# Optimization experiments

Hardware: AMD Instinct MI355X
Metric: run time of the kernel (lower is better)

Reference implementation:

```python
import jax, jax.numpy as jnp
import numpy as np

HIDDEN = 768

def setup_inputs() -> dict:
    key = jax.random.key(0)
    ks = jax.random.split(key, 7)
    x = jax.random.normal(ks[0], (4, 4096, HIDDEN), dtype=jnp.float32)
    s = 1.0 / np.sqrt(HIDDEN)
    Wq = jax.random.uniform(ks[1], (HIDDEN, HIDDEN), minval=-s, maxval=s, dtype=jnp.float32)
    Wk = jax.random.uniform(ks[2], (HIDDEN, HIDDEN), minval=-s, maxval=s, dtype=jnp.float32)
    Wv = jax.random.uniform(ks[3], (HIDDEN, HIDDEN), minval=-s, maxval=s, dtype=jnp.float32)
    bq = jax.random.uniform(ks[4], (HIDDEN,), minval=-s, maxval=s, dtype=jnp.float32)
    bk = jax.random.uniform(ks[5], (HIDDEN,), minval=-s, maxval=s, dtype=jnp.float32)
    bv = jax.random.uniform(ks[6], (HIDDEN,), minval=-s, maxval=s, dtype=jnp.float32)
    return {"x": x, "Wq": Wq, "bq": bq, "Wk": Wk, "bk": bk, "Wv": Wv, "bv": bv}

def reference(x, Wq, bq, Wk, bk, Wv, bv):
    # q,k,v: [b, s, d]
    q = jnp.einsum('bsd,de->bse', x, Wq.T) + bq
    k = jnp.einsum('bsd,de->bse', x, Wk.T) + bk
    v = jnp.einsum('bsd,de->bse', x, Wv.T) + bv
    scale = 1.0 / jnp.sqrt(jnp.asarray(x.shape[-1], dtype=x.dtype))
    scores = jnp.einsum('bqd,bkd->bqk', q, k) * scale  # [b, s, s]
    attn = jax.nn.softmax(scores, axis=-1)
    return jnp.einsum('bqk,bkd->bqd', attn, v)
```

## Files before the change

kernel.cpp:

```cpp
#include <hip/hip_runtime.h>
#include <stdint.h>

typedef unsigned short u16;
typedef __attribute__((ext_vector_type(8))) short    bf16x8;
typedef __attribute__((ext_vector_type(4))) float    f32x4;

__device__ __forceinline__ u16 f2bf(float f) {
    unsigned u = __float_as_uint(f);
    u = (u + 0x7fffu + ((u >> 16) & 1u)) >> 16;
    return (u16)u;
}

__global__ __launch_bounds__(256) void cast_bf16_kernel(const float* __restrict__ in,
                                                        u16* __restrict__ out, int n4) {
    int i = blockIdx.x * 256 + threadIdx.x;
    if (i < n4) {
        float4 f = ((const float4*)in)[i];
        ushort4 o;
        o.x = f2bf(f.x); o.y = f2bf(f.y); o.z = f2bf(f.z); o.w = f2bf(f.w);
        ((ushort4*)out)[i] = o;
    }
}

__global__ __launch_bounds__(256) void cast3_bf16_kernel(const float* __restrict__ w0,
                                                         const float* __restrict__ w1,
                                                         const float* __restrict__ w2,
                                                         u16* __restrict__ out) {
    const float* src = (blockIdx.y == 0) ? w0 : (blockIdx.y == 1) ? w1 : w2;
    int i = blockIdx.x * 256 + threadIdx.x;
    float4 f = ((const float4*)src)[i];
    ushort4 o;
    o.x = f2bf(f.x); o.y = f2bf(f.y); o.z = f2bf(f.z); o.w = f2bf(f.w);
    ((ushort4*)out)[(size_t)blockIdx.y * 147456 + i] = o;
}

__global__ __launch_bounds__(256) void transpose_bf16_kernel(const u16* __restrict__ V,
                                                             u16* __restrict__ Vt,
                                                             float* __restrict__ rsum) {
    __shared__ u16 tile[32][33];
    const int t = threadIdx.x;
    if (blockIdx.x == 0 && blockIdx.z == 0) {
        int idx = blockIdx.y * 256 + t;
        if (idx < 16384) rsum[idx] = 0.f;
    }
    const size_t z = blockIdx.z;
    const u16* Vb  = V  + z * (size_t)4096 * 2304;
    u16*       Vtb = Vt + z * (size_t)768 * 4096;
    const int c0 = blockIdx.x * 32;
    const int r0 = blockIdx.y * 32;
    const int lr = t >> 3;
    const int lc = (t & 7) * 4;
    ushort4 in = *(const ushort4*)&Vb[(size_t)(r0 + lr) * 2304 + c0 + lc];
    tile[lr][lc + 0] = in.x; tile[lr][lc + 1] = in.y;
    tile[lr][lc + 2] = in.z; tile[lr][lc + 3] = in.w;
    __syncthreads();
    ushort4 o;
    o.x = tile[lc + 0][lr]; o.y = tile[lc + 1][lr];
    o.z = tile[lc + 2][lr]; o.w = tile[lc + 3][lr];
    *(ushort4*)&Vtb[(size_t)(c0 + lr) * 4096 + r0 + lc] = o;
}

template <int EPI, int WN, int NBX, int GRP, int NGRID, int NBY, int MINW>
__global__ __launch_bounds__(256, MINW) void gemm_bt_kernel(
        const u16* __restrict__ A, const u16* __restrict__ B, void* __restrict__ Cv,
        const float* __restrict__ b0, const float* __restrict__ b1, const float* __restrict__ b2,
        float* __restrict__ rs, float s2, int K,
        int lda, int ldb, int ldc, long batchA, long batchB, long batchC) {
    __shared__ __align__(16) u16 As[128 * 64];
    __shared__ __align__(16) u16 Bs[32 * WN * 64];

    constexpr int SPX = NGRID / (8 * NBX);
    const int lin = blockIdx.x;
    const int c = lin & 7, p = lin >> 3;
    const int bxi = p % GRP;
    const int rest = p / GRP;
    const int s = rest % SPX;
    const int g = rest / SPX;
    const int bx = g * GRP + bxi;
    const int strip = c * SPX + s;
    const int by = strip % NBY;
    const int bz = strip / NBY;

    const int t = threadIdx.x;
    const long z = bz;
    const u16* Ab = A + z * batchA + (long)by * 128 * lda;
    const u16* Bb = B + z * batchB + (long)bx * (32 * WN) * ldb;

    const int lane = t & 63;
    const int wave = t >> 6;
    const int wm = wave >> 1, wn = wave & 1;
    const int quad = lane >> 4;
    const int frow = lane & 15;
    const int cc0 = quad ^ (frow & 7);

    f32x4 acc[4][WN];
#pragma unroll
    for (int i = 0; i < 4; i++)
#pragma unroll
        for (int j = 0; j < WN; j++)
#pragma unroll
            for (int e = 0; e < 4; e++) acc[i][j][e] = 0.f;

    int srow[WN], scol[WN];
#pragma unroll
    for (int j = 0; j < WN; j++) {
        const int d = t + j * 256;
        srow[j] = d >> 3;
        scol[j] = ((d & 7) ^ (srow[j] & 7)) * 8;
    }

    bf16x8 ra[4], rb[WN];
#pragma unroll
    for (int j = 0; j < 4; j++)
        ra[j] = *(const bf16x8*)(Ab + (long)srow[j] * lda + scol[j]);
#pragma unroll
    for (int j = 0; j < WN; j++)
        rb[j] = *(const bf16x8*)(Bb + (long)srow[j] * ldb + scol[j]);

    for (int kt = 0; kt < K; kt += 64) {
#pragma unroll
        for (int j = 0; j < 4; j++)
            *(bf16x8*)&As[(t + j * 256) * 8] = ra[j];
#pragma unroll
        for (int j = 0; j < WN; j++)
            *(bf16x8*)&Bs[(t + j * 256) * 8] = rb[j];
        __syncthreads();

        if (kt + 64 < K) {
            const int kn = kt + 64;
#pragma unroll
            for (int j = 0; j < 4; j++)
                ra[j] = *(const bf16x8*)(Ab + (long)srow[j] * lda + kn + scol[j]);
#pragma unroll
            for (int j = 0; j < WN; j++)
                rb[j] = *(const bf16x8*)(Bb + (long)srow[j] * ldb + kn + scol[j]);
        }

#pragma unroll
        for (int kk = 0; kk < 2; kk++) {
            const int cc = (cc0 ^ (kk * 4)) * 8;
            bf16x8 bfr[WN];
#pragma unroll
            for (int j = 0; j < WN; j++)
                bfr[j] = *(const bf16x8*)&Bs[(wn * WN * 16 + j * 16 + frow) * 64 + cc];
#pragma unroll
            for (int i = 0; i < 4; i++) {
                bf16x8 af = *(const bf16x8*)&As[(wm * 64 + i * 16 + frow) * 64 + cc];
#pragma unroll
                for (int j = 0; j < WN; j++)
                    acc[i][j] = __builtin_amdgcn_mfma_f32_16x16x32_bf16(af, bfr[j], acc[i][j], 0, 0, 0);
            }
        }
        __syncthreads();
    }

    const int m_base = by * 128 + wm * 64;
    const int n_base = bx * (32 * WN) + wn * (16 * WN);

    if (EPI == 0) {
        const int seg = n_base / 768;
        const float* bp = (seg == 0) ? b0 : (seg == 1) ? b1 : b2;
        u16* C = (u16*)Cv + z * batchC;
#pragma unroll
        for (int j = 0; j < WN; j++) {
            const int col = n_base + j * 16 + frow;
            const float bb = bp[col - seg * 768];
#pragma unroll
            for (int i = 0; i < 4; i++) {
                const int row0 = m_base + i * 16 + quad * 4;
#pragma unroll
                for (int r = 0; r < 4; r++)
                    C[(long)(row0 + r) * ldc + col] = f2bf(acc[i][j][r] + bb);
            }
        }
    } else if (EPI == 1) {
        u16* C = (u16*)Cv + z * batchC;
        float rowpart[4][4];
#pragma unroll
        for (int i = 0; i < 4; i++)
#pragma unroll
            for (int r = 0; r < 4; r++) rowpart[i][r] = 0.f;
#pragma unroll
        for (int i = 0; i < 4; i++) {
            const int row0 = m_base + i * 16 + quad * 4;
#pragma unroll
            for (int j = 0; j < WN; j++) {
                const int col = n_base + j * 16 + frow;
#pragma unroll
                for (int r = 0; r < 4; r++) {
                    float e = exp2f(acc[i][j][r] * s2);
                    C[(long)(row0 + r) * ldc + col] = f2bf(e);
                    rowpart[i][r] += e;
                }
            }
        }
#pragma unroll
        for (int i = 0; i < 4; i++)
#pragma unroll
            for (int r = 0; r < 4; r++) {
                float v = rowpart[i][r];
                v += __shfl_xor(v, 1); v += __shfl_xor(v, 2);
                v += __shfl_xor(v, 4); v += __shfl_xor(v, 8);
                if (frow == 0)
                    atomicAdd(&rs[z * 4096 + m_base + i * 16 + quad * 4 + r], v);
            }
    } else {
        float* C = (float*)Cv + z * batchC;
#pragma unroll
        for (int i = 0; i < 4; i++) {
            const int row0 = m_base + i * 16 + quad * 4;
            float inv[4];
#pragma unroll
            for (int r = 0; r < 4; r++) inv[r] = 1.0f / rs[z * 4096 + row0 + r];
#pragma unroll
            for (int j = 0; j < WN; j++) {
                const int col = n_base + j * 16 + frow;
#pragma unroll
                for (int r = 0; r < 4; r++)
                    C[(long)(row0 + r) * ldc + col] = acc[i][j][r] * inv[r];
            }
        }
    }
}

__device__ __forceinline__ void gload16(const u16* src, u16* dst) {
    __builtin_amdgcn_global_load_lds((const __attribute__((address_space(1))) void*)src,
                                     (__attribute__((address_space(3))) void*)dst,
                                     16, 0, 0);
}

template <int EPI, int NBX, int NBY, int NT>
__global__ __launch_bounds__(512, 2) void gemm8_kernel(
        const u16* __restrict__ A, const u16* __restrict__ B, void* __restrict__ Cv,
        float* __restrict__ rs, float s2,
        int lda, int ldb, int ldc, long batchA, long batchB, long batchC) {
    static_assert(NT >= 3, "pipeline needs >=3 K-tiles");
    __shared__ __align__(16) u16 lds[2][4][8192];

    constexpr int NWG = NBX * NBY * 4;
    const int lin = blockIdx.x;
    const int swz = (lin & 7) * (NWG / 8) + (lin >> 3);
    const int bz  = swz / (NBX * NBY);
    const int rr_ = swz % (NBX * NBY);
    const int by  = rr_ / NBX, bx = rr_ % NBX;

    const int t_   = threadIdx.x;
    const int lane = t_ & 63;
    const int wave = t_ >> 6;
    const int wm = wave >> 2, wn = wave & 3;
    const int frow = lane & 15, quad = lane >> 4;

    const u16* Ab = A + (long)bz * batchA + (long)by * 256 * lda;
    const u16* Bb = B + (long)bz * batchB + (long)bx * 256 * ldb;

    const int srow = ((t_ >> 3) << 1) | ((t_ >> 2) & 1);
    const int scol = ((t_ & 3) ^ ((t_ >> 3) & 3)) * 8;
    const int dstu = wave * 512;

    const int rdoff = (frow >> 1) * 64
                    + ((frow & 1) * 4 + (quad ^ ((frow >> 1) & 3))) * 8;
    const int aoff = wm * 128 * 32 + rdoff;
    const int boff = wn * 64 * 32 + rdoff;

    f32x4 acc[8][4];
#pragma unroll
    for (int i = 0; i < 8; i++)
#pragma unroll
        for (int j = 0; j < 4; j++)
#pragma unroll
            for (int e = 0; e < 4; e++) acc[i][j][e] = 0.f;

    auto STAGE = [&](int buf, int reg, const u16* gb, int ld_, int kofs) {
#pragma unroll
        for (int j = 0; j < 2; ++j) {
            const u16* sp = gb + (long)(srow + j * 128) * ld_ + kofs + scol;
            gload16(sp, &lds[buf][reg][dstu + j * 4096]);
        }
    };

    STAGE(0, 2, Bb, ldb, 0);
    STAGE(0, 0, Ab, lda, 0);
    STAGE(0, 3, Bb, ldb, 32);
    STAGE(0, 1, Ab, lda, 32);
    STAGE(1, 2, Bb, ldb, 64);
    STAGE(1, 0, Ab, lda, 64);
    STAGE(1, 3, Bb, ldb, 96);
    asm volatile("s_waitcnt vmcnt(6)" ::: "memory");
    __builtin_amdgcn_s_barrier();

#define MFMA16(SUB)                                                              \
    __builtin_amdgcn_s_setprio(1);                                               \
    _Pragma("unroll")                                                            \
    for (int i = 0; i < 4; ++i)                                                  \
        _Pragma("unroll")                                                        \
        for (int j = 0; j < 4; ++j)                                              \
            acc[(SUB) * 4 + i][j] = __builtin_amdgcn_mfma_f32_16x16x32_bf16(     \
                a[i], b[j], acc[(SUB) * 4 + i][j], 0, 0, 0);                     \
    __builtin_amdgcn_s_setprio(0);

#pragma unroll 2
    for (int t = 0; t < NT; ++t) {
        const int cur = t & 1, nxt = cur ^ 1;
        const u16* A0 = (const u16*)lds[cur][0];
        const u16* A1 = (const u16*)lds[cur][1];
        const u16* B0 = (const u16*)lds[cur][2];
        const u16* B1 = (const u16*)lds[cur][3];
        bf16x8 a[4], b[4];

#pragma unroll
        for (int i = 0; i < 4; ++i) a[i] = *(const bf16x8*)&A0[aoff + i * 512];
#pragma unroll
        for (int j = 0; j < 4; ++j) b[j] = *(const bf16x8*)&B0[boff + j * 512];
        if (t + 1 < NT) STAGE(nxt, 1, Ab, lda, (t + 1) * 64 + 32);
        __builtin_amdgcn_s_barrier();
        asm volatile("s_waitcnt lgkmcnt(0)" ::: "memory");
        MFMA16(0)
        __builtin_amdgcn_s_barrier();

#pragma unroll
        for (int i = 0; i < 4; ++i) a[i] = *(const bf16x8*)&A0[aoff + 2048 + i * 512];
        if (t + 2 < NT) STAGE(cur, 2, Bb, ldb, (t + 2) * 64);
        __builtin_amdgcn_s_barrier();
        asm volatile("s_waitcnt lgkmcnt(0)" ::: "memory");
        MFMA16(1)
        __builtin_amdgcn_s_barrier();

#pragma unroll
        for (int i = 0; i < 4; ++i) a[i] = *(const bf16x8*)&A1[aoff + i * 512];
#pragma unroll
        for (int j = 0; j < 4; ++j) b[j] = *(const bf16x8*)&B1[boff + j * 512];
        if (t + 2 < NT) STAGE(cur, 0, Ab, lda, (t + 2) * 64);
        __builtin_amdgcn_s_barrier();
        asm volatile("s_waitcnt lgkmcnt(0)" ::: "memory");
        MFMA16(0)
        __builtin_amdgcn_s_barrier();

#pragma unroll
        for (int i = 0; i < 4; ++i) a[i] = *(const bf16x8*)&A1[aoff + 2048 + i * 512];
        if (t + 2 < NT) STAGE(cur, 3, Bb, ldb, (t + 2) * 64 + 32);
        __builtin_amdgcn_s_barrier();
        asm volatile("s_waitcnt lgkmcnt(0)" ::: "memory");
        MFMA16(1)
        if (t + 2 < NT)      asm volatile("s_waitcnt vmcnt(6)" ::: "memory");
        else if (t + 1 < NT) asm volatile("s_waitcnt vmcnt(0)" ::: "memory");
        __builtin_amdgcn_s_barrier();
    }
#undef MFMA16

    const int m_base = by * 256 + wm * 128;
    const int n_base = bx * 256 + wn * 64;
    const long z = bz;

    if (EPI == 1) {
        u16* C = (u16*)Cv + z * batchC;
#pragma unroll
        for (int ig = 0; ig < 8; ++ig) {
            const int row0 = m_base + ig * 16 + quad * 4;
            float rp[4] = {0.f, 0.f, 0.f, 0.f};
#pragma unroll
            for (int j = 0; j < 4; ++j) {
                const int col = n_base + j * 16 + frow;
#pragma unroll
                for (int r = 0; r < 4; ++r) {
                    float e = exp2f(acc[ig][j][r] * s2);
                    C[(long)(row0 + r) * ldc + col] = f2bf(e);
                    rp[r] += e;
                }
            }
#pragma unroll
            for (int r = 0; r < 4; ++r) {
                float v = rp[r];
                v += __shfl_xor(v, 1); v += __shfl_xor(v, 2);
                v += __shfl_xor(v, 4); v += __shfl_xor(v, 8);
                if (frow == 0) atomicAdd(&rs[z * 4096 + row0 + r], v);
            }
        }
    } else {
        float* C = (float*)Cv + z * batchC;
#pragma unroll
        for (int ig = 0; ig < 8; ++ig) {
            const int row0 = m_base + ig * 16 + quad * 4;
            float inv[4];
#pragma unroll
            for (int r = 0; r < 4; ++r) inv[r] = 1.0f / rs[z * 4096 + row0 + r];
#pragma unroll
            for (int j = 0; j < 4; ++j) {
                const int col = n_base + j * 16 + frow;
#pragma unroll
                for (int r = 0; r < 4; ++r)
                    C[(long)(row0 + r) * ldc + col] = acc[ig][j][r] * inv[r];
            }
        }
    }
}

extern "C" void kernel_launch(void* const* d_in, const int* in_sizes, int n_in,
                              void* d_out, int out_size, void* d_ws, size_t ws_size,
                              hipStream_t stream) {
    const float* x  = (const float*)d_in[0];
    const float* Wq = (const float*)d_in[1];
    const float* bq = (const float*)d_in[2];
    const float* Wk = (const float*)d_in[3];
    const float* bk = (const float*)d_in[4];
    const float* Wv = (const float*)d_in[5];
    const float* bv = (const float*)d_in[6];
    float* out = (float*)d_out;

    uint8_t* ws = (uint8_t*)d_ws;
    u16*   xb   = (u16*)(ws + 0);
    u16*   Vt   = (u16*)(ws + 0);
    u16*   QKV  = (u16*)(ws + 25165824);
    u16*   E    = (u16*)(ws + 100663296);
    u16*   Wqkv = (u16*)(ws + 234881024);
    float* rsum = (float*)(ws + 234881024);

    cast_bf16_kernel<<<12288, 256, 0, stream>>>(x, xb, 3145728);
    cast3_bf16_kernel<<<dim3(576, 3), 256, 0, stream>>>(Wq, Wk, Wv, Wqkv);

    gemm_bt_kernel<0, 4, 18, 6, 2304, 128, 3><<<2304, 256, 0, stream>>>(
        xb, Wqkv, QKV, bq, bk, bv, nullptr, 0.f, 768, 768, 768, 2304, 0, 0, 0);

    transpose_bf16_kernel<<<dim3(24, 128, 4), 256, 0, stream>>>(QKV + 1536, Vt, rsum);

    gemm8_kernel<1, 16, 16, 12><<<1024, 512, 0, stream>>>(
        QKV, QKV + 768, E, rsum, 0.05205954822032348f,
        2304, 2304, 4096, (long)4096 * 2304, (long)4096 * 2304, (long)4096 * 4096);

    gemm8_kernel<2, 3, 16, 64><<<192, 512, 0, stream>>>(
        E, Vt, out, rsum, 0.f,
        4096, 4096, 768, (long)4096 * 4096, (long)768 * 4096, (long)4096 * 768);
}
```

Baseline: 439.0 us.

## Fuse cast kernels, remap gemm8 tiles, use inline-asm LDS reads, swap PV GEMM

Merges the x and weight bf16 cast kernels into a single launch to save one kernel launch. Replaces the gemm8 block swizzle with a grouped mapping (GRP columns per strip, strips spread across the 8 XCDs) meant to improve L2 reuse. Switches the LDS fragment reads to inline-asm ds_read_b128 with immediate offsets, and adds sched_barrier so MFMAs are not hoisted above the waits. Runs the P·V GEMM with gemm_bt_kernel on a 768-block grid instead of gemm8 on 192 blocks, to get more parallelism across CUs.

Result: faster. 414.6 us, median of 2 (-5.6%).

```diff
diff --git a/kernel.cpp b/kernel.cpp
--- a/kernel.cpp
+++ b/kernel.cpp
@@ -11,27 +11,30 @@
     return (u16)u;
 }
 
-__global__ __launch_bounds__(256) void cast_bf16_kernel(const float* __restrict__ in,
-                                                        u16* __restrict__ out, int n4) {
-    int i = blockIdx.x * 256 + threadIdx.x;
-    if (i < n4) {
-        float4 f = ((const float4*)in)[i];
+__global__ __launch_bounds__(256) void cast_all_kernel(const float* __restrict__ x,
+                                                       const float* __restrict__ w0,
+                                                       const float* __restrict__ w1,
+                                                       const float* __restrict__ w2,
+                                                       u16* __restrict__ xb,
+                                                       u16* __restrict__ wb) {
+    const int b = blockIdx.x;
+    if (b < 12288) {
+        int i = b * 256 + threadIdx.x;
+        float4 f = ((const float4*)x)[i];
         ushort4 o;
         o.x = f2bf(f.x); o.y = f2bf(f.y); o.z = f2bf(f.z); o.w = f2bf(f.w);
-        ((ushort4*)out)[i] = o;
-    }
-}
-
-__global__ __launch_bounds__(256) void cast3_bf16_kernel(const float* __restrict__ w0,
-                                                         const float* __restrict__ w1,
-                                                         const float* __restrict__ w2,
-                                                         u16* __restrict__ out) {
-    const float* src = (blockIdx.y == 0) ? w0 : (blockIdx.y == 1) ? w1 : w2;
-    int i = blockIdx.x * 256 + threadIdx.x;
-    float4 f = ((const float4*)src)[i];
-    ushort4 o;
-    o.x = f2bf(f.x); o.y = f2bf(f.y); o.z = f2bf(f.z); o.w = f2bf(f.w);
-    ((ushort4*)out)[(size_t)blockIdx.y * 147456 + i] = o;
+        ((ushort4*)xb)[i] = o;
+    } else {
+        const int i2 = b - 12288;
+        const int w  = i2 / 576;
+        const int blk = i2 - w * 576;
+        const float* src = (w == 0) ? w0 : (w == 1) ? w1 : w2;
+        int i = blk * 256 + threadIdx.x;
+        float4 f = ((const float4*)src)[i];
+        ushort4 o;
+        o.x = f2bf(f.x); o.y = f2bf(f.y); o.z = f2bf(f.z); o.w = f2bf(f.w);
+        ((ushort4*)wb)[(size_t)w * 147456 + i] = o;
+    }
 }
 
 __global__ __launch_bounds__(256) void transpose_bf16_kernel(const u16* __restrict__ V,
@@ -229,20 +232,35 @@
                                      16, 0, 0);
 }
 
-template <int EPI, int NBX, int NBY, int NT>
+template <int IMM>
+__device__ __forceinline__ bf16x8 dsr128(uint32_t addr) {
+    bf16x8 r;
+    asm volatile("ds_read_b128 %0, %1 offset:%2" : "=v"(r) : "v"(addr), "i"(IMM));
+    return r;
+}
+
+#define LDS_ADDR(BUF, REG) \
+    ((uint32_t)(uintptr_t)(__attribute__((address_space(3))) void*)&lds[BUF][REG][0])
+
+template <int EPI, int NBX, int NBY, int GRP, int NGRID, int NT>
 __global__ __launch_bounds__(512, 2) void gemm8_kernel(
         const u16* __restrict__ A, const u16* __restrict__ B, void* __restrict__ Cv,
         float* __restrict__ rs, float s2,
         int lda, int ldb, int ldc, long batchA, long batchB, long batchC) {
-    static_assert(NT >= 3, "pipeline needs >=3 K-tiles");
+    static_assert(NT >= 3 && (NT % 2) == 0, "pipeline needs even NT >= 4");
     __shared__ __align__(16) u16 lds[2][4][8192];
 
-    constexpr int NWG = NBX * NBY * 4;
+    constexpr int SPX = NGRID / (8 * NBX);
     const int lin = blockIdx.x;
-    const int swz = (lin & 7) * (NWG / 8) + (lin >> 3);
-    const int bz  = swz / (NBX * NBY);
-    const int rr_ = swz % (NBX * NBY);
-    const int by  = rr_ / NBX, bx = rr_ % NBX;
+    const int c = lin & 7, p = lin >> 3;
+    const int bxi = p % GRP;
+    const int rest = p / GRP;
+    const int s = rest % SPX;
+    const int g = rest / SPX;
+    const int bx = g * GRP + bxi;
+    const int strip = c * SPX + s;
+    const int by = strip % NBY;
+    const int bz = strip / NBY;
 
     const int t_   = threadIdx.x;
     const int lane = t_ & 63;
@@ -257,10 +275,10 @@
     const int scol = ((t_ & 3) ^ ((t_ >> 3) & 3)) * 8;
     const int dstu = wave * 512;
 
-    const int rdoff = (frow >> 1) * 64
-                    + ((frow & 1) * 4 + (quad ^ ((frow >> 1) & 3))) * 8;
-    const int aoff = wm * 128 * 32 + rdoff;
-    const int boff = wn * 64 * 32 + rdoff;
+    const uint32_t rdoff2 = (uint32_t)(((frow >> 1) * 64
+                          + ((frow & 1) * 4 + (quad ^ ((frow >> 1) & 3))) * 8) * 2);
+    const uint32_t aoff2 = (uint32_t)(wm * 128 * 32 * 2) + rdoff2;
+    const uint32_t boff2 = (uint32_t)(wn * 64 * 32 * 2) + rdoff2;
 
     f32x4 acc[8][4];
 #pragma unroll
@@ -298,54 +316,66 @@
                 a[i], b[j], acc[(SUB) * 4 + i][j], 0, 0, 0);                     \
     __builtin_amdgcn_s_setprio(0);
 
+#define SYNC_PRE_MFMA()                                      \
+    __builtin_amdgcn_s_barrier();                            \
+    asm volatile("s_waitcnt lgkmcnt(0)" ::: "memory");       \
+    __builtin_amdgcn_sched_barrier(0);
+
 #pragma unroll 2
     for (int t = 0; t < NT; ++t) {
         const int cur = t & 1, nxt = cur ^ 1;
-        const u16* A0 = (const u16*)lds[cur][0];
-        const u16* A1 = (const u16*)lds[cur][1];
-        const u16* B0 = (const u16*)lds[cur][2];
-        const u16* B1 = (const u16*)lds[cur][3];
         bf16x8 a[4], b[4];
 
-#pragma unroll
-        for (int i = 0; i < 4; ++i) a[i] = *(const bf16x8*)&A0[aoff + i * 512];
-#pragma unroll
-        for (int j = 0; j < 4; ++j) b[j] = *(const bf16x8*)&B0[boff + j * 512];
+        {
+            const uint32_t aA = LDS_ADDR(cur, 0) + aoff2;
+            const uint32_t aB = LDS_ADDR(cur, 2) + boff2;
+            a[0] = dsr128<0>(aA);    a[1] = dsr128<1024>(aA);
+            a[2] = dsr128<2048>(aA); a[3] = dsr128<3072>(aA);
+            b[0] = dsr128<0>(aB);    b[1] = dsr128<1024>(aB);
+            b[2] = dsr128<2048>(aB); b[3] = dsr128<3072>(aB);
+        }
         if (t + 1 < NT) STAGE(nxt, 1, Ab, lda, (t + 1) * 64 + 32);
-        __builtin_amdgcn_s_barrier();
-        asm volatile("s_waitcnt lgkmcnt(0)" ::: "memory");
+        SYNC_PRE_MFMA()
         MFMA16(0)
         __builtin_amdgcn_s_barrier();
 
-#pragma unroll
-        for (int i = 0; i < 4; ++i) a[i] = *(const bf16x8*)&A0[aoff + 2048 + i * 512];
+        {
+            const uint32_t aA = LDS_ADDR(cur, 0) + aoff2;
+            a[0] = dsr128<4096>(aA); a[1] = dsr128<5120>(aA);
+            a[2] = dsr128<6144>(aA); a[3] = dsr128<7168>(aA);
+        }
         if (t + 2 < NT) STAGE(cur, 2, Bb, ldb, (t + 2) * 64);
-        __builtin_amdgcn_s_barrier();
-        asm volatile("s_waitcnt lgkmcnt(0)" ::: "memory");
+        SYNC_PRE_MFMA()
         MFMA16(1)
         __builtin_amdgcn_s_barrier();
 
-#pragma unroll
-        for (int i = 0; i < 4; ++i) a[i] = *(const bf16x8*)&A1[aoff + i * 512];
-#pragma unroll
-        for (int j = 0; j < 4; ++j) b[j] = *(const bf16x8*)&B1[boff + j * 512];
+        {
+            const uint32_t aA = LDS_ADDR(cur, 1) + aoff2;
+            const uint32_t aB = LDS_ADDR(cur, 3) + boff2;
+            a[0] = dsr128<0>(aA);    a[1] = dsr128<1024>(aA);
+            a[2] = dsr128<2048>(aA); a[3] = dsr128<3072>(aA);
+            b[0] = dsr128<0>(aB);    b[1] = dsr128<1024>(aB);
+            b[2] = dsr128<2048>(aB); b[3] = dsr128<3072>(aB);
+        }
         if (t + 2 < NT) STAGE(cur, 0, Ab, lda, (t + 2) * 64);
-        __builtin_amdgcn_s_barrier();
-        asm volatile("s_waitcnt lgkmcnt(0)" ::: "memory");
+        SYNC_PRE_MFMA()
         MFMA16(0)
         __builtin_amdgcn_s_barrier();
 
-#pragma unroll
-        for (int i = 0; i < 4; ++i) a[i] = *(const bf16x8*)&A1[aoff + 2048 + i * 512];
+        {
+            const uint32_t aA = LDS_ADDR(cur, 1) + aoff2;
+            a[0] = dsr128<4096>(aA); a[1] = dsr128<5120>(aA);
+            a[2] = dsr128<6144>(aA); a[3] = dsr128<7168>(aA);
+        }
         if (t + 2 < NT) STAGE(cur, 3, Bb, ldb, (t + 2) * 64 + 32);
-        __builtin_amdgcn_s_barrier();
-        asm volatile("s_waitcnt lgkmcnt(0)" ::: "memory");
+        SYNC_PRE_MFMA()
         MFMA16(1)
         if (t + 2 < NT)      asm volatile("s_waitcnt vmcnt(6)" ::: "memory");
         else if (t + 1 < NT) asm volatile("s_waitcnt vmcnt(0)" ::: "memory");
         __builtin_amdgcn_s_barrier();
     }
 #undef MFMA16
+#undef SYNC_PRE_MFMA
 
     const int m_base = by * 256 + wm * 128;
     const int n_base = bx * 256 + wn * 64;
@@ -414,19 +444,18 @@
     u16*   Wqkv = (u16*)(ws + 234881024);
     float* rsum = (float*)(ws + 234881024);
 
-    cast_bf16_kernel<<<12288, 256, 0, stream>>>(x, xb, 3145728);
-    cast3_bf16_kernel<<<dim3(576, 3), 256, 0, stream>>>(Wq, Wk, Wv, Wqkv);
+    cast_all_kernel<<<14016, 256, 0, stream>>>(x, Wq, Wk, Wv, xb, Wqkv);
 
     gemm_bt_kernel<0, 4, 18, 6, 2304, 128, 3><<<2304, 256, 0, stream>>>(
         xb, Wqkv, QKV, bq, bk, bv, nullptr, 0.f, 768, 768, 768, 2304, 0, 0, 0);
 
     transpose_bf16_kernel<<<dim3(24, 128, 4), 256, 0, stream>>>(QKV + 1536, Vt, rsum);
 
-    gemm8_kernel<1, 16, 16, 12><<<1024, 512, 0, stream>>>(
+    gemm8_kernel<1, 16, 16, 4, 1024, 12><<<1024, 512, 0, stream>>>(
         QKV, QKV + 768, E, rsum, 0.05205954822032348f,
         2304, 2304, 4096, (long)4096 * 2304, (long)4096 * 2304, (long)4096 * 4096);
 
-    gemm8_kernel<2, 3, 16, 64><<<192, 512, 0, stream>>>(
-        E, Vt, out, rsum, 0.f,
-        4096, 4096, 768, (long)4096 * 4096, (long)768 * 4096, (long)4096 * 768);
-}
+    gemm_bt_kernel<2, 4, 6, 6, 768, 32, 3><<<768, 256, 0, stream>>>(
+        E, Vt, out, nullptr, nullptr, nullptr, rsum, 0.f,
+        4096, 4096, 4096, 768, (long)4096 * 4096, (long)768 * 4096, (long)4096 * 768);
+}
```
